# Performance work log

Hardware: AMD Instinct MI355X
Metric: run time of the kernel (lower is better)

Reference implementation:

```python
import jax, jax.numpy as jnp
import numpy as np

N, M, D, S = 4, 256, 32, 32


def setup_inputs() -> dict:
    key = jax.random.key(0)
    k1, k2 = jax.random.split(key)
    inputs = jax.random.normal(k1, (N, M, M, D), dtype=jnp.float32)
    mask = jnp.ones((N, M, 1), dtype=bool)
    coeffs = jax.random.normal(k2, (D, S, 15), dtype=jnp.float32) * np.sqrt(2.0) / (D + S)
    diag_bias = jnp.zeros((1, S, 1, 1), dtype=jnp.float32)
    all_bias = jnp.zeros((1, S, 1, 1), dtype=jnp.float32)
    return {"inputs": inputs, "mask": mask, "coeffs": coeffs,
            "diag_bias": diag_bias, "all_bias": all_bias}


def _contractions_2_to_2(x):
    # x: [N, D, m, m]; returns list of 15 [N, D, m, m] basis tensors ('inf' normalization)
    n, d, m, _ = x.shape
    diag = jnp.diagonal(x, axis1=2, axis2=3)            # [N, D, m]
    sum_diag = jnp.sum(diag, axis=2, keepdims=True)      # [N, D, 1]
    rows = jnp.sum(x, axis=3)                            # [N, D, m]
    cols = jnp.sum(x, axis=2)                            # [N, D, m]
    tot = jnp.sum(rows, axis=2)                          # [N, D]
    eye = jnp.eye(m, dtype=x.dtype)

    def diag_embed(v):  # v: [N, D, m] -> [N, D, m, m]
        return v[..., :, None] * eye

    full = x.shape
    op1 = diag_embed(diag)
    op2 = diag_embed(jnp.broadcast_to(sum_diag, diag.shape)) / m
    op3 = diag_embed(rows) / m
    op4 = diag_embed(cols) / m
    op5 = diag_embed(jnp.broadcast_to(tot[..., None], diag.shape)) / (m ** 2)
    op6 = jnp.broadcast_to(cols[..., :, None], full) / m
    op7 = jnp.broadcast_to(rows[..., :, None], full) / m
    op8 = jnp.broadcast_to(cols[..., None, :], full) / m
    op9 = jnp.broadcast_to(rows[..., None, :], full) / m
    op10 = x
    op11 = jnp.swapaxes(x, 2, 3)
    op12 = jnp.broadcast_to(diag[..., :, None], full)
    op13 = jnp.broadcast_to(diag[..., None, :], full)
    op14 = jnp.broadcast_to(sum_diag[..., None], full) / m
    op15 = jnp.broadcast_to(tot[..., None, None], full) / (m ** 2)
    return [op1, op2, op3, op4, op5, op6, op7, op8, op9, op10,
            op11, op12, op13, op14, op15]


def reference(inputs, mask, coeffs, diag_bias, all_bias):
    # inputs: [N, m, m, D] -> [N, D, m, m]
    x = jnp.transpose(inputs, (0, 3, 1, 2))
    m = x.shape[3]
    ops = _contractions_2_to_2(x)
    # einsum('dsb,ndbij->nsij') expressed as accumulation over the 15 bases
    # (avoids materializing the [N, D, 15, m, m] stack)
    out = jnp.zeros((x.shape[0], coeffs.shape[1], m, m), dtype=x.dtype)
    for b, op in enumerate(ops):
        out = out + jnp.einsum('ds,ndij->nsij', coeffs[:, :, b], op)
    eye = jnp.eye(m, dtype=x.dtype)[None, None]
    out = out + all_bias + eye * diag_bias
    return jnp.transpose(out, (0, 2, 3, 1))  # [N, m, m, S]
```

## Files before the change

### kernel.cpp

```cpp
#include <hip/hip_runtime.h>


#define NN 4
#define MM 256
#define DD 32
#define SS 32

#define WS_COLS   0
#define WS_SD     32768
#define WS_TOT    32896
#define WS_ROWS   33024
#define WS_DIAG   65792
#define WS_RW     98560
#define WS_CWT    131328
#define WS_DW     164096
#define WS_CPACK  196864

__global__ __launch_bounds__(256) void k_rows(const float* __restrict__ in,
                                              float* __restrict__ ws) {
    int nm = blockIdx.x;
    int n = nm >> 8;
    int ii = nm & 255;
    int t = threadIdx.x;
    const float4* base = (const float4*)(in + (size_t)nm * MM * DD);
    float4 a = {0.f, 0.f, 0.f, 0.f};
    #pragma unroll
    for (int k = 0; k < 8; ++k) {
        float4 v = base[t + k * 256];
        a.x += v.x; a.y += v.y; a.z += v.z; a.w += v.w;
    }
    __shared__ float4 red[256];
    red[t] = a;
    __syncthreads();
    if (t < 8) {
        float4 s = {0.f, 0.f, 0.f, 0.f};
        #pragma unroll 8
        for (int g = 0; g < 32; ++g) {
            float4 v = red[g * 8 + t];
            s.x += v.x; s.y += v.y; s.z += v.z; s.w += v.w;
        }
        ((float4*)(ws + WS_ROWS))[nm * 8 + t] = s;
        float4 dv = ((const float4*)in)[((size_t)nm * MM + ii) * 8 + t];
        ((float4*)(ws + WS_DIAG))[nm * 8 + t] = dv;
        atomicAdd(ws + WS_TOT + n * DD + t * 4 + 0, s.x);
        atomicAdd(ws + WS_TOT + n * DD + t * 4 + 1, s.y);
        atomicAdd(ws + WS_TOT + n * DD + t * 4 + 2, s.z);
        atomicAdd(ws + WS_TOT + n * DD + t * 4 + 3, s.w);
        atomicAdd(ws + WS_SD + n * DD + t * 4 + 0, dv.x);
        atomicAdd(ws + WS_SD + n * DD + t * 4 + 1, dv.y);
        atomicAdd(ws + WS_SD + n * DD + t * 4 + 2, dv.z);
        atomicAdd(ws + WS_SD + n * DD + t * 4 + 3, dv.w);
    }
}

__global__ __launch_bounds__(256) void k_cols(const float* __restrict__ in,
                                              const float* __restrict__ coeffs,
                                              float* __restrict__ ws) {
    int b = blockIdx.x;
    int t = threadIdx.x;
    if (b < 256) {
        int n = b >> 6, jb = (b >> 3) & 7, ic = b & 7;
        int i0 = ic * 32, j0 = jb * 32;
        const float4* base = (const float4*)in
            + ((size_t)(n * MM + i0) * MM + j0) * 8 + t;
        float4 a0 = {0,0,0,0}, a1 = {0,0,0,0}, a2 = {0,0,0,0}, a3 = {0,0,0,0};
        #pragma unroll 4
        for (int i = 0; i < 32; i += 4) {
            float4 v0 = base[(size_t)(i + 0) * MM * 8];
            float4 v1 = base[(size_t)(i + 1) * MM * 8];
            float4 v2 = base[(size_t)(i + 2) * MM * 8];
            float4 v3 = base[(size_t)(i + 3) * MM * 8];
            a0.x += v0.x; a0.y += v0.y; a0.z += v0.z; a0.w += v0.w;
            a1.x += v1.x; a1.y += v1.y; a1.z += v1.z; a1.w += v1.w;
            a2.x += v2.x; a2.y += v2.y; a2.z += v2.z; a2.w += v2.w;
            a3.x += v3.x; a3.y += v3.y; a3.z += v3.z; a3.w += v3.w;
        }
        float4 a = {a0.x + a1.x + a2.x + a3.x, a0.y + a1.y + a2.y + a3.y,
                    a0.z + a1.z + a2.z + a3.z, a0.w + a1.w + a2.w + a3.w};
        int j = j0 + (t >> 3), d = (t & 7) * 4;
        float* dst = ws + WS_COLS + (n * MM + j) * DD + d;
        atomicAdd(dst + 0, a.x);
        atomicAdd(dst + 1, a.y);
        atomicAdd(dst + 2, a.z);
        atomicAdd(dst + 3, a.w);
    } else {
        for (int idx = t; idx < 15 * DD * SS; idx += 256) {
            int plane = idx >> 10;
            int ds = idx & 1023;
            ws[WS_CPACK + plane * (DD * SS) + ds] = coeffs[ds * 15 + plane];
        }
    }
}

__global__ __launch_bounds__(256) void k_aux(const float* __restrict__ diag_bias,
                                             const float* __restrict__ all_bias,
                                             float* __restrict__ ws) {
    int idx = blockIdx.x * blockDim.x + threadIdx.x;
    int s = idx & 31;
    int nm = idx >> 5;
    int n = nm >> 8;
    int m = nm & 255;
    const float inv_m = 1.0f / MM;
    const float inv_m2 = inv_m * inv_m;
    float u = 0.f, v = 0.f, dgacc = 0.f, w = 0.f;
    for (int d = 0; d < DD; ++d) {
        const float* cp = ws + WS_CPACK + d * SS + s;
        float r = ws[WS_ROWS + nm * DD + d];
        float cl = ws[WS_COLS + nm * DD + d];
        float dv = ws[WS_DIAG + nm * DD + d];
        float sdv = ws[WS_SD + n * DD + d];
        float totv = ws[WS_TOT + n * DD + d];
        u += cp[5 * 1024] * cl * inv_m + cp[6 * 1024] * r * inv_m + cp[11 * 1024] * dv;
        v += cp[7 * 1024] * cl * inv_m + cp[8 * 1024] * r * inv_m + cp[12 * 1024] * dv;
        dgacc += cp[0] * dv + cp[1 * 1024] * sdv * inv_m + cp[2 * 1024] * r * inv_m
               + cp[3 * 1024] * cl * inv_m + cp[4 * 1024] * totv * inv_m2;
        w += cp[13 * 1024] * sdv * inv_m + cp[14 * 1024] * totv * inv_m2;
    }
    ws[WS_RW + nm * SS + s] = u + w + all_bias[s];
    ws[WS_CWT + (n * SS + s) * MM + m] = v;
    ws[WS_DW + nm * SS + s] = dgacc + diag_bias[s];
}

__global__ __launch_bounds__(256) void k_main(const float* __restrict__ in,
                                              const float* __restrict__ ws,
                                              float* __restrict__ out) {
    __shared__ float tile[256 * 36];
    int nm = blockIdx.x;
    int n = nm >> 8;
    int i = nm & 255;
    int t = threadIdx.x;

    const float* rwp = ws + WS_RW + nm * SS;
    const float* cwt = ws + WS_CWT + n * SS * MM + t;
    float acc[SS];
    #pragma unroll
    for (int s = 0; s < SS; ++s) acc[s] = rwp[s] + cwt[s * MM];
    if (t == i) {
        const float4* dw = (const float4*)(ws + WS_DW + nm * SS);
        #pragma unroll
        for (int q = 0; q < 8; ++q) {
            float4 dq = dw[q];
            acc[q * 4 + 0] += dq.x;
            acc[q * 4 + 1] += dq.y;
            acc[q * 4 + 2] += dq.z;
            acc[q * 4 + 3] += dq.w;
        }
    }

    {
        const float4* Arow = (const float4*)(in + (size_t)nm * MM * DD);
        #pragma unroll
        for (int k = 0; k < 8; ++k) {
            int idx = t + k * 256;
            int p = idx >> 3, c = idx & 7;
            float4 v = Arow[idx];
            *(float4*)(tile + p * 36 + c * 4) = v;
        }
    }
    __syncthreads();

    const float* c10 = ws + WS_CPACK + 9 * (DD * SS);
    const float* c11 = ws + WS_CPACK + 10 * (DD * SS);
    const float* lrow = tile + t * 36;
    #pragma unroll
    for (int dq = 0; dq < 8; ++dq) {
        float4 a4 = *(const float4*)(lrow + dq * 4);
        const float* ca = c10 + dq * 4 * SS;
        #pragma unroll
        for (int r = 0; r < 4; ++r) {
            float a = (r == 0) ? a4.x : (r == 1) ? a4.y : (r == 2) ? a4.z : a4.w;
            #pragma unroll
            for (int s = 0; s < SS; ++s)
                acc[s] = fmaf(a, ca[r * SS + s], acc[s]);
        }
    }
    __syncthreads();

    {
        const float4* Bbase = (const float4*)in;
        #pragma unroll
        for (int k = 0; k < 8; ++k) {
            int idx = t + k * 256;
            int p = idx >> 3, c = idx & 7;
            float4 v = Bbase[((size_t)(n * MM + p) * MM + i) * 8 + c];
            *(float4*)(tile + p * 36 + c * 4) = v;
        }
    }
    __syncthreads();

    #pragma unroll
    for (int dq = 0; dq < 8; ++dq) {
        float4 b4 = *(const float4*)(lrow + dq * 4);
        const float* cb = c11 + dq * 4 * SS;
        #pragma unroll
        for (int r = 0; r < 4; ++r) {
            float bb = (r == 0) ? b4.x : (r == 1) ? b4.y : (r == 2) ? b4.z : b4.w;
            #pragma unroll
            for (int s = 0; s < SS; ++s)
                acc[s] = fmaf(bb, cb[r * SS + s], acc[s]);
        }
    }
    #pragma unroll
    for (int q = 0; q < 8; ++q)
        *(float4*)(tile + t * 36 + q * 4) =
            make_float4(acc[q * 4 + 0], acc[q * 4 + 1], acc[q * 4 + 2], acc[q * 4 + 3]);
    __syncthreads();

    {
        float4* Orow = (float4*)(out + (size_t)nm * MM * SS);
        #pragma unroll
        for (int k = 0; k < 8; ++k) {
            int idx = t + k * 256;
            int p = idx >> 3, c = idx & 7;
            Orow[idx] = *(const float4*)(tile + p * 36 + c * 4);
        }
    }
}

extern "C" void kernel_launch(void* const* d_in, const int* in_sizes, int n_in,
                              void* d_out, int out_size, void* d_ws, size_t ws_size,
                              hipStream_t stream) {
    const float* in = (const float*)d_in[0];
    const float* coeffs = (const float*)d_in[2];
    const float* diag_bias = (const float*)d_in[3];
    const float* all_bias = (const float*)d_in[4];
    float* out = (float*)d_out;
    float* ws = (float*)d_ws;

    hipMemsetAsync(d_ws, 0, (size_t)(32768 + 256) * sizeof(float), stream);
    k_rows<<<NN * MM, 256, 0, stream>>>(in, ws);
    k_cols<<<257, 256, 0, stream>>>(in, coeffs, ws);
    k_aux<<<(NN * MM * SS) / 256, 256, 0, stream>>>(diag_bias, all_bias, ws);
    k_main<<<NN * MM, 256, 0, stream>>>(in, ws, out);
}
```

Baseline: 160.1 us.

## Merge row/col reductions into one kernel and prefetch both input tiles in main

Fuses the row-sum and column-sum kernels into a single launch. Column partials are written per i-chunk and summed in the aux kernel instead of using atomics, which also shrinks the memset. The column-weight buffer is laid out as float4 groups so the main kernel can load it vectorized. The main kernel issues the A-row and transposed B-column global loads up front into registers before any LDS staging, so the strided B gather overlaps the first FMA phase. The cost is higher register pressure, an extra 1 MB partial buffer, and eight reads per column value in k_aux.

```diff
diff --git a/kernel.cpp b/kernel.cpp
--- a/kernel.cpp
+++ b/kernel.cpp
@@ -6,83 +6,67 @@
 #define DD 32
 #define SS 32
 
-#define WS_COLS   0
-#define WS_SD     32768
-#define WS_TOT    32896
-#define WS_ROWS   33024
-#define WS_DIAG   65792
-#define WS_RW     98560
-#define WS_CWT    131328
-#define WS_DW     164096
-#define WS_CPACK  196864
-
-__global__ __launch_bounds__(256) void k_rows(const float* __restrict__ in,
-                                              float* __restrict__ ws) {
-    int nm = blockIdx.x;
-    int n = nm >> 8;
-    int ii = nm & 255;
+#define WS_COLSP  0
+#define WS_ROWS   262144
+#define WS_DIAG   294912
+#define WS_SD     327680
+#define WS_TOT    327808
+#define WS_RW     327936
+#define WS_CWT4   360704
+#define WS_DW     393472
+#define WS_CPACK  426240
+
+__global__ __launch_bounds__(256) void k_reduce(const float* __restrict__ in,
+                                                const float* __restrict__ coeffs,
+                                                float* __restrict__ ws) {
+    int blk = blockIdx.x;
     int t = threadIdx.x;
-    const float4* base = (const float4*)(in + (size_t)nm * MM * DD);
-    float4 a = {0.f, 0.f, 0.f, 0.f};
-    #pragma unroll
-    for (int k = 0; k < 8; ++k) {
-        float4 v = base[t + k * 256];
-        a.x += v.x; a.y += v.y; a.z += v.z; a.w += v.w;
-    }
-    __shared__ float4 red[256];
-    red[t] = a;
-    __syncthreads();
-    if (t < 8) {
-        float4 s = {0.f, 0.f, 0.f, 0.f};
+    if (blk < 256) {
+        int n = blk >> 6, rem = blk & 63, jb = rem >> 3, ie = rem & 7;
+        int i0 = ie * 32, j0 = jb * 32;
+        int jl = t >> 3, d4 = t & 7;
+        const float4* base = (const float4*)in
+            + ((size_t)(n * MM + i0) * MM + j0 + jl) * 8 + d4;
+        float4 a = {0.f, 0.f, 0.f, 0.f};
         #pragma unroll 8
-        for (int g = 0; g < 32; ++g) {
-            float4 v = red[g * 8 + t];
-            s.x += v.x; s.y += v.y; s.z += v.z; s.w += v.w;
-        }
-        ((float4*)(ws + WS_ROWS))[nm * 8 + t] = s;
-        float4 dv = ((const float4*)in)[((size_t)nm * MM + ii) * 8 + t];
-        ((float4*)(ws + WS_DIAG))[nm * 8 + t] = dv;
-        atomicAdd(ws + WS_TOT + n * DD + t * 4 + 0, s.x);
-        atomicAdd(ws + WS_TOT + n * DD + t * 4 + 1, s.y);
-        atomicAdd(ws + WS_TOT + n * DD + t * 4 + 2, s.z);
-        atomicAdd(ws + WS_TOT + n * DD + t * 4 + 3, s.w);
-        atomicAdd(ws + WS_SD + n * DD + t * 4 + 0, dv.x);
-        atomicAdd(ws + WS_SD + n * DD + t * 4 + 1, dv.y);
-        atomicAdd(ws + WS_SD + n * DD + t * 4 + 2, dv.z);
-        atomicAdd(ws + WS_SD + n * DD + t * 4 + 3, dv.w);
-    }
-}
-
-__global__ __launch_bounds__(256) void k_cols(const float* __restrict__ in,
-                                              const float* __restrict__ coeffs,
-                                              float* __restrict__ ws) {
-    int b = blockIdx.x;
-    int t = threadIdx.x;
-    if (b < 256) {
-        int n = b >> 6, jb = (b >> 3) & 7, ic = b & 7;
-        int i0 = ic * 32, j0 = jb * 32;
-        const float4* base = (const float4*)in
-            + ((size_t)(n * MM + i0) * MM + j0) * 8 + t;
-        float4 a0 = {0,0,0,0}, a1 = {0,0,0,0}, a2 = {0,0,0,0}, a3 = {0,0,0,0};
-        #pragma unroll 4
-        for (int i = 0; i < 32; i += 4) {
-            float4 v0 = base[(size_t)(i + 0) * MM * 8];
-            float4 v1 = base[(size_t)(i + 1) * MM * 8];
-            float4 v2 = base[(size_t)(i + 2) * MM * 8];
-            float4 v3 = base[(size_t)(i + 3) * MM * 8];
-            a0.x += v0.x; a0.y += v0.y; a0.z += v0.z; a0.w += v0.w;
-            a1.x += v1.x; a1.y += v1.y; a1.z += v1.z; a1.w += v1.w;
-            a2.x += v2.x; a2.y += v2.y; a2.z += v2.z; a2.w += v2.w;
-            a3.x += v3.x; a3.y += v3.y; a3.z += v3.z; a3.w += v3.w;
-        }
-        float4 a = {a0.x + a1.x + a2.x + a3.x, a0.y + a1.y + a2.y + a3.y,
-                    a0.z + a1.z + a2.z + a3.z, a0.w + a1.w + a2.w + a3.w};
-        int j = j0 + (t >> 3), d = (t & 7) * 4;
-        float* dst = ws + WS_COLS + (n * MM + j) * DD + d;
-        atomicAdd(dst + 0, a.x);
-        atomicAdd(dst + 1, a.y);
-        atomicAdd(dst + 2, a.z);
-        atomicAdd(dst + 3, a.w);
+        for (int i = 0; i < 32; ++i) {
+            float4 v = base[(size_t)i * MM * 8];
+            a.x += v.x; a.y += v.y; a.z += v.z; a.w += v.w;
+        }
+        ((float4*)(ws + WS_COLSP))[(size_t)ie * 8192 + (n * MM + j0 + jl) * 8 + d4] = a;
+    } else if (blk < 256 + NN * MM) {
+        int nm = blk - 256;
+        int n = nm >> 8;
+        int ii = nm & 255;
+        const float4* base = (const float4*)(in + (size_t)nm * MM * DD);
+        float4 a = {0.f, 0.f, 0.f, 0.f};
+        #pragma unroll
+        for (int k = 0; k < 8; ++k) {
+            float4 v = base[t + k * 256];
+            a.x += v.x; a.y += v.y; a.z += v.z; a.w += v.w;
+        }
+        __shared__ float4 red[256];
+        red[t] = a;
+        __syncthreads();
+        if (t < 8) {
+            float4 s = {0.f, 0.f, 0.f, 0.f};
+            #pragma unroll 8
+            for (int g = 0; g < 32; ++g) {
+                float4 v = red[g * 8 + t];
+                s.x += v.x; s.y += v.y; s.z += v.z; s.w += v.w;
+            }
+            ((float4*)(ws + WS_ROWS))[nm * 8 + t] = s;
+            float4 dv = ((const float4*)in)[((size_t)nm * MM + ii) * 8 + t];
+            ((float4*)(ws + WS_DIAG))[nm * 8 + t] = dv;
+            atomicAdd(ws + WS_TOT + n * DD + t * 4 + 0, s.x);
+            atomicAdd(ws + WS_TOT + n * DD + t * 4 + 1, s.y);
+            atomicAdd(ws + WS_TOT + n * DD + t * 4 + 2, s.z);
+            atomicAdd(ws + WS_TOT + n * DD + t * 4 + 3, s.w);
+            atomicAdd(ws + WS_SD + n * DD + t * 4 + 0, dv.x);
+            atomicAdd(ws + WS_SD + n * DD + t * 4 + 1, dv.y);
+            atomicAdd(ws + WS_SD + n * DD + t * 4 + 2, dv.z);
+            atomicAdd(ws + WS_SD + n * DD + t * 4 + 3, dv.w);
+        }
     } else {
         for (int idx = t; idx < 15 * DD * SS; idx += 256) {
             int plane = idx >> 10;
@@ -106,7 +90,9 @@
     for (int d = 0; d < DD; ++d) {
         const float* cp = ws + WS_CPACK + d * SS + s;
         float r = ws[WS_ROWS + nm * DD + d];
-        float cl = ws[WS_COLS + nm * DD + d];
+        float cl = 0.f;
+        #pragma unroll
+        for (int q = 0; q < 8; ++q) cl += ws[WS_COLSP + q * 32768 + nm * DD + d];
         float dv = ws[WS_DIAG + nm * DD + d];
         float sdv = ws[WS_SD + n * DD + d];
         float totv = ws[WS_TOT + n * DD + d];
@@ -117,7 +103,7 @@
         w += cp[13 * 1024] * sdv * inv_m + cp[14 * 1024] * totv * inv_m2;
     }
     ws[WS_RW + nm * SS + s] = u + w + all_bias[s];
-    ws[WS_CWT + (n * SS + s) * MM + m] = v;
+    ws[WS_CWT4 + (((n * 8 + (s >> 2)) * MM + m) << 2) + (s & 3)] = v;
     ws[WS_DW + nm * SS + s] = dgacc + diag_bias[s];
 }
 
@@ -130,34 +116,49 @@
     int i = nm & 255;
     int t = threadIdx.x;
 
-    const float* rwp = ws + WS_RW + nm * SS;
-    const float* cwt = ws + WS_CWT + n * SS * MM + t;
-    float acc[SS];
-    #pragma unroll
-    for (int s = 0; s < SS; ++s) acc[s] = rwp[s] + cwt[s * MM];
+    const float4* Arow = (const float4*)(in + (size_t)nm * MM * DD);
+    float4 avv[8];
+    #pragma unroll
+    for (int k = 0; k < 8; ++k) avv[k] = Arow[t + k * 256];
+
+    float4 cvv[8];
+    const float4* cwt4 = (const float4*)(ws + WS_CWT4) + (size_t)n * 8 * MM + t;
+    #pragma unroll
+    for (int sq = 0; sq < 8; ++sq) cvv[sq] = cwt4[sq * MM];
+    float4 dvv[8] = {};
     if (t == i) {
         const float4* dw = (const float4*)(ws + WS_DW + nm * SS);
         #pragma unroll
-        for (int q = 0; q < 8; ++q) {
-            float4 dq = dw[q];
-            acc[q * 4 + 0] += dq.x;
-            acc[q * 4 + 1] += dq.y;
-            acc[q * 4 + 2] += dq.z;
-            acc[q * 4 + 3] += dq.w;
-        }
-    }
-
-    {
-        const float4* Arow = (const float4*)(in + (size_t)nm * MM * DD);
-        #pragma unroll
-        for (int k = 0; k < 8; ++k) {
-            int idx = t + k * 256;
-            int p = idx >> 3, c = idx & 7;
-            float4 v = Arow[idx];
-            *(float4*)(tile + p * 36 + c * 4) = v;
-        }
-    }
-    __syncthreads();
+        for (int q = 0; q < 8; ++q) dvv[q] = dw[q];
+    }
+
+    const float4* Bbase = (const float4*)in;
+    float4 bvv[8];
+    #pragma unroll
+    for (int k = 0; k < 8; ++k) {
+        int idx = t + k * 256;
+        int p = idx >> 3, c = idx & 7;
+        bvv[k] = Bbase[((size_t)(n * MM + p) * MM + i) * 8 + c];
+    }
+    __builtin_amdgcn_sched_barrier(0);
+
+    #pragma unroll
+    for (int k = 0; k < 8; ++k) {
+        int idx = t + k * 256;
+        int p = idx >> 3, c = idx & 7;
+        *(float4*)(tile + p * 36 + c * 4) = avv[k];
+    }
+    __syncthreads();
+
+    const float* rwp = ws + WS_RW + nm * SS;
+    float acc[SS];
+    #pragma unroll
+    for (int sq = 0; sq < 8; ++sq) {
+        acc[sq * 4 + 0] = rwp[sq * 4 + 0] + cvv[sq].x + dvv[sq].x;
+        acc[sq * 4 + 1] = rwp[sq * 4 + 1] + cvv[sq].y + dvv[sq].y;
+        acc[sq * 4 + 2] = rwp[sq * 4 + 2] + cvv[sq].z + dvv[sq].z;
+        acc[sq * 4 + 3] = rwp[sq * 4 + 3] + cvv[sq].w + dvv[sq].w;
+    }
 
     const float* c10 = ws + WS_CPACK + 9 * (DD * SS);
     const float* c11 = ws + WS_CPACK + 10 * (DD * SS);
@@ -176,15 +177,11 @@
     }
     __syncthreads();
 
-    {
-        const float4* Bbase = (const float4*)in;
-        #pragma unroll
-        for (int k = 0; k < 8; ++k) {
-            int idx = t + k * 256;
-            int p = idx >> 3, c = idx & 7;
-            float4 v = Bbase[((size_t)(n * MM + p) * MM + i) * 8 + c];
-            *(float4*)(tile + p * 36 + c * 4) = v;
-        }
+    #pragma unroll
+    for (int k = 0; k < 8; ++k) {
+        int idx = t + k * 256;
+        int p = idx >> 3, c = idx & 7;
+        *(float4*)(tile + p * 36 + c * 4) = bvv[k];
     }
     __syncthreads();
 
@@ -206,14 +203,12 @@
             make_float4(acc[q * 4 + 0], acc[q * 4 + 1], acc[q * 4 + 2], acc[q * 4 + 3]);
     __syncthreads();
 
-    {
-        float4* Orow = (float4*)(out + (size_t)nm * MM * SS);
-        #pragma unroll
-        for (int k = 0; k < 8; ++k) {
-            int idx = t + k * 256;
-            int p = idx >> 3, c = idx & 7;
-            Orow[idx] = *(const float4*)(tile + p * 36 + c * 4);
-        }
+    float4* Orow = (float4*)(out + (size_t)nm * MM * SS);
+    #pragma unroll
+    for (int k = 0; k < 8; ++k) {
+        int idx = t + k * 256;
+        int p = idx >> 3, c = idx & 7;
+        Orow[idx] = *(const float4*)(tile + p * 36 + c * 4);
     }
 }
 
@@ -227,9 +222,8 @@
     float* out = (float*)d_out;
     float* ws = (float*)d_ws;
 
-    hipMemsetAsync(d_ws, 0, (size_t)(32768 + 256) * sizeof(float), stream);
-    k_rows<<<NN * MM, 256, 0, stream>>>(in, ws);
-    k_cols<<<257, 256, 0, stream>>>(in, coeffs, ws);
+    hipMemsetAsync((char*)d_ws + (size_t)WS_SD * 4, 0, 256 * sizeof(float), stream);
+    k_reduce<<<256 + NN * MM + 1, 256, 0, stream>>>(in, coeffs, ws);
     k_aux<<<(NN * MM * SS) / 256, 256, 0, stream>>>(diag_bias, all_bias, ws);
     k_main<<<NN * MM, 256, 0, stream>>>(in, ws, out);
 }
```

Result: slower. 165.9 us (+3.6%).
